# Kernel optimization log

Hardware: AMD Instinct MI355X
Metric: run time of the kernel (lower is better)

The kernel has to match this reference:

```python
import jax, jax.numpy as jnp
import numpy as np

H = W = 32
V = 1.5  # gaussian sigma used by the original _gussin(1.5)

def _gaussian_table():
    # gus[p, x, y] with p = i*32 + k, matching the original nested loops.
    r = np.arange(H, dtype=np.float64)
    d = (r[:, None, None, None] - r[None, None, :, None]) ** 2 \
        + (r[None, :, None, None] - r[None, None, None, :]) ** 2  # [i,k,x,y]
    g = np.exp(-d / (2.0 * V * V)) / (2.0 * np.pi * V * V)
    g = g.reshape(H * W, H, W)
    g = g / g.sum(axis=(1, 2), keepdims=True)  # per-position boundary normalization
    return jnp.asarray(g, dtype=jnp.float32)

_GUS = _gaussian_table()  # [1024, 32, 32]

def setup_inputs() -> dict:
    key = jax.random.key(0)
    ks = jax.random.split(key, 5)
    c, r = 1024, 16
    return {
        "x": jax.random.normal(ks[0], (1, c, H, W), jnp.float32),
        "se_w1": jax.random.normal(ks[1], (c // r, c), jnp.float32) * 0.03,
        "se_b1": jnp.zeros((c // r,), jnp.float32),
        "se_w2": jax.random.normal(ks[2], (c, c // r), jnp.float32) * 0.1,
        "se_b2": jnp.zeros((c,), jnp.float32),
        "conv_w": jax.random.normal(ks[3], (c, 2 * c), jnp.float32) * 0.02,
        "bn_gamma": jnp.ones((c,), jnp.float32),
        "bn_beta": jnp.zeros((c,), jnp.float32),
        "bn_mean": jnp.zeros((c,), jnp.float32),
        "bn_var": jnp.ones((c,), jnp.float32),
    }

def reference(x, se_w1, se_b1, se_w2, se_b2, conv_w, bn_gamma, bn_beta, bn_mean, bn_var):
    b, c, h, w = x.shape  # b == 1, h == w == 32 (hardcoded by the gaussian table)
    # ---- SE block ----
    y = x.mean(axis=(2, 3))                              # [b, c]
    y = jax.nn.relu(y @ se_w1.T + se_b1)                 # [b, c//r]
    y = jax.nn.sigmoid(y @ se_w2.T + se_b2)              # [b, c]
    x = x * y[:, :, None, None]
    # ---- gaussian spatial pooling (algebraic form of the O(H^2 W^2 C) expand) ----
    # x_spatial[c, p] = sum_{h,w} x[c,h,w] * gus[p,h,w]
    x_spatial = jnp.einsum('chw,phw->cp', x[0], _GUS).reshape(c, h, w)
    # ---- 3x3 local softmax attention on sigmoid features ----
    xr = jax.nn.sigmoid(x)                               # [1, c, h, w]
    xp = jnp.pad(xr, ((0, 0), (0, 0), (1, 1), (1, 1)))
    # torch F.unfold ordering: feature index = c_idx*9 + kh*3 + kw
    patches = jnp.stack([xp[:, :, i:i + h, j:j + w]
                         for i in range(3) for j in range(3)], axis=2)  # [1, c, 9, h, w]
    u = patches.reshape(c * 9, h * w).T                  # [hw, c*9]
    # faithful to the original reshape(hw, 3, 3, c) (reinterprets the c*9 layout)
    x3 = u.reshape(h * w, 3, 3, c)
    x1 = xr[0].transpose(1, 2, 0).reshape(h * w, 1, 1, c)
    logits = (x1 * x3).sum(-1).reshape(h * w, 9)         # [hw, 9]
    attn = jax.nn.softmax(logits, axis=1).reshape(h * w, 3, 3)
    x_range = jnp.einsum('pij,pijc->cp', attn, x3).reshape(c, h, w)
    # ---- fuse: 1x1 conv (no bias) + eval-mode BatchNorm + ReLU ----
    cat = jnp.concatenate([x_range, x_spatial], axis=0).reshape(b, 2 * c, h, w)
    out = jnp.einsum('oc,bchw->bohw', conv_w, cat)
    inv = jax.lax.rsqrt(bn_var + 1e-5)
    out = (out - bn_mean[None, :, None, None]) * (inv * bn_gamma)[None, :, None, None] \
          + bn_beta[None, :, None, None]
    return jax.nn.relu(out)
```

## Files before the change

kernel.cpp:

```cpp
#include <hip/hip_runtime.h>
#include <hip/hip_bf16.h>


typedef __attribute__((ext_vector_type(8))) short v8s;
typedef __attribute__((ext_vector_type(4))) float v4f;

__device__ __forceinline__ float sigmoidf_(float v) {
    return 1.f / (1.f + __expf(-v));
}
__device__ __forceinline__ unsigned short f2bf(float f) {
    unsigned u = __float_as_uint(f);
    u += 0x7fffu + ((u >> 16) & 1u);
    return (unsigned short)(u >> 16);
}
__device__ __forceinline__ float bf2f(unsigned short s) {
    return __uint_as_float(((unsigned)s) << 16);
}

__global__ __launch_bounds__(256) void k_A(const float* __restrict__ x,
                                           const float* __restrict__ W,
                                           const float* __restrict__ w1,
                                           const float* __restrict__ gamma,
                                           const float* __restrict__ beta,
                                           const float* __restrict__ mu,
                                           const float* __restrict__ var,
                                           unsigned short* __restrict__ Wb,
                                           unsigned short* __restrict__ U,
                                           float* __restrict__ zpart,
                                           float* __restrict__ bnsc,
                                           float* __restrict__ bnsh) {
    __shared__ unsigned short Gb[32 * 48];
    __shared__ unsigned short Xs[4][32 * 48];
    __shared__ unsigned short Ts[4][32 * 48];
    __shared__ float ms4[4];
    int tid = threadIdx.x, bx = blockIdx.x;
    int wv = tid >> 6, lane = tid & 63;
    {
        int row = tid >> 3, col0 = (tid & 7) << 2;
        float e[4], s = 0.f;
        #pragma unroll
        for (int j = 0; j < 4; ++j) {
            float d = (float)(row - (col0 + j));
            e[j] = __expf(-d * d / 4.5f);
            s += e[j];
        }
        s += __shfl_xor(s, 4, 8);
        s += __shfl_xor(s, 2, 8);
        s += __shfl_xor(s, 1, 8);
        float is = 1.f / s;
        uint2 pk;
        pk.x = (unsigned)f2bf(e[0] * is) | ((unsigned)f2bf(e[1] * is) << 16);
        pk.y = (unsigned)f2bf(e[2] * is) | ((unsigned)f2bf(e[3] * is) << 16);
        *(uint2*)&Gb[row * 48 + col0] = pk;
    }
    #pragma unroll
    for (int k = 0; k < 8; ++k) {
        int e = (k << 18) + (bx << 10) + (tid << 2);
        float4 v = *(const float4*)(W + e);
        uint2 pk;
        pk.x = (unsigned)f2bf(v.x) | ((unsigned)f2bf(v.y) << 16);
        pk.y = (unsigned)f2bf(v.z) | ((unsigned)f2bf(v.w) << 16);
        *(uint2*)(Wb + e) = pk;
    }
    int c = (bx << 2) + wv;
    if (lane == 0) {
        float iv = rsqrtf(var[c] + 1e-5f);
        float sc = iv * gamma[c];
        bnsc[c] = sc;
        bnsh[c] = beta[c] - mu[c] * sc;
    }
    const float* xp = x + (size_t)c * 1024;
    float4 vj[4];
    float s = 0.f;
    #pragma unroll
    for (int j = 0; j < 4; ++j) {
        vj[j] = *(const float4*)(xp + (j << 8) + (lane << 2));
        s += vj[j].x + vj[j].y + vj[j].z + vj[j].w;
    }
    #pragma unroll
    for (int o = 32; o; o >>= 1) s += __shfl_down(s, o);
    if (lane == 0) ms4[wv] = s * (1.f / 1024.f);
    #pragma unroll
    for (int j = 0; j < 4; ++j) {
        int h = (j << 3) + (lane >> 3);
        int w0 = (lane & 7) << 2;
        uint2 pk;
        pk.x = (unsigned)f2bf(vj[j].x) | ((unsigned)f2bf(vj[j].y) << 16);
        pk.y = (unsigned)f2bf(vj[j].z) | ((unsigned)f2bf(vj[j].w) << 16);
        *(uint2*)&Xs[wv][h * 48 + w0] = pk;
    }
    __syncthreads();
    int colf = lane & 15, quad = lane >> 4;
    v8s ga[2], xbv[2];
    #pragma unroll
    for (int mi = 0; mi < 2; ++mi)
        ga[mi] = *(const v8s*)&Gb[(mi * 16 + colf) * 48 + quad * 8];
    #pragma unroll
    for (int ni = 0; ni < 2; ++ni)
        xbv[ni] = *(const v8s*)&Xs[wv][(ni * 16 + colf) * 48 + quad * 8];
    v4f c1[2][2];
    #pragma unroll
    for (int mi = 0; mi < 2; ++mi)
        #pragma unroll
        for (int ni = 0; ni < 2; ++ni) {
            c1[mi][ni] = (v4f){0.f, 0.f, 0.f, 0.f};
            c1[mi][ni] = __builtin_amdgcn_mfma_f32_16x16x32_bf16(ga[mi], xbv[ni], c1[mi][ni], 0, 0, 0);
        }
    #pragma unroll
    for (int mi = 0; mi < 2; ++mi)
        #pragma unroll
        for (int ni = 0; ni < 2; ++ni)
            #pragma unroll
            for (int r = 0; r < 4; ++r)
                Ts[wv][(mi * 16 + quad * 4 + r) * 48 + ni * 16 + colf] = f2bf(c1[mi][ni][r]);
    __syncthreads();
    v8s tb[2];
    #pragma unroll
    for (int ni = 0; ni < 2; ++ni)
        tb[ni] = *(const v8s*)&Ts[wv][(ni * 16 + colf) * 48 + quad * 8];
    v4f c2[2][2];
    #pragma unroll
    for (int mi = 0; mi < 2; ++mi)
        #pragma unroll
        for (int ni = 0; ni < 2; ++ni) {
            c2[mi][ni] = (v4f){0.f, 0.f, 0.f, 0.f};
            c2[mi][ni] = __builtin_amdgcn_mfma_f32_16x16x32_bf16(ga[mi], tb[ni], c2[mi][ni], 0, 0, 0);
        }
    #pragma unroll
    for (int mi = 0; mi < 2; ++mi)
        #pragma unroll
        for (int ni = 0; ni < 2; ++ni)
            #pragma unroll
            for (int r = 0; r < 4; ++r)
                U[(size_t)c * 1024 + (mi * 16 + quad * 4 + r) * 32 + ni * 16 + colf] =
                    f2bf(c2[mi][ni][r]);
    if (wv == 0) {
        float4 wr = *(const float4*)(w1 + (size_t)lane * 1024 + (bx << 2));
        zpart[lane * 256 + bx] = wr.x * ms4[0] + wr.y * ms4[1]
                               + wr.z * ms4[2] + wr.w * ms4[3];
    }
}

__global__ __launch_bounds__(256) void k_prep(const float* __restrict__ x,
                                              const float* __restrict__ zpart,
                                              const float* __restrict__ b1,
                                              const float* __restrict__ w2,
                                              const float* __restrict__ b2,
                                              const unsigned short* __restrict__ U,
                                              unsigned short* __restrict__ xrb,
                                              unsigned short* __restrict__ Bt) {
    __shared__ float y1s[64];
    __shared__ float y2s[64];
    __shared__ float T[64][65];
    int tid = threadIdx.x;
    int p0 = blockIdx.x << 6, c0 = blockIdx.y << 6;
    {
        int j = tid >> 2, q = tid & 3;
        const float4* zp = (const float4*)(zpart + j * 256 + q * 64);
        float s = 0.f;
        #pragma unroll
        for (int i = 0; i < 16; ++i) {
            float4 v = zp[i];
            s += v.x + v.y + v.z + v.w;
        }
        s += __shfl_down(s, 2, 4);
        s += __shfl_down(s, 1, 4);
        if (q == 0) y1s[j] = fmaxf(s + b1[j], 0.f);
    }
    __syncthreads();
    {
        int ci = tid >> 2, sub = tid & 3;
        float s = 0.f;
        const float* w2r = w2 + (size_t)(c0 + ci) * 64 + sub * 16;
        #pragma unroll
        for (int i = 0; i < 4; ++i) {
            float4 wv4 = *(const float4*)(w2r + (i << 2));
            float4 yv4 = *(const float4*)&y1s[sub * 16 + (i << 2)];
            s += wv4.x * yv4.x + wv4.y * yv4.y + wv4.z * yv4.z + wv4.w * yv4.w;
        }
        s += __shfl_down(s, 2, 4);
        s += __shfl_down(s, 1, 4);
        if (sub == 0) y2s[ci] = sigmoidf_(s + b2[c0 + ci]);
    }
    __syncthreads();
    #pragma unroll
    for (int i = 0; i < 4; ++i) {
        int idx = tid + (i << 8);
        int row = idx >> 4;
        int col = (idx & 15) << 2;
        float sc = y2s[row];
        float4 v = *(const float4*)(x + (size_t)(c0 + row) * 1024 + p0 + col);
        T[col + 0][row] = sigmoidf_(v.x * sc);
        T[col + 1][row] = sigmoidf_(v.y * sc);
        T[col + 2][row] = sigmoidf_(v.z * sc);
        T[col + 3][row] = sigmoidf_(v.w * sc);
    }
    __syncthreads();
    #pragma unroll
    for (int i = 0; i < 4; ++i) {
        int idx = tid + (i << 8);
        int prow = idx >> 4;
        int cc = (idx & 15) << 2;
        uint2 pk;
        pk.x = (unsigned)f2bf(T[prow][cc + 0]) | ((unsigned)f2bf(T[prow][cc + 1]) << 16);
        pk.y = (unsigned)f2bf(T[prow][cc + 2]) | ((unsigned)f2bf(T[prow][cc + 3]) << 16);
        *(uint2*)(xrb + (size_t)(p0 + prow) * 1024 + c0 + cc) = pk;
    }
    __syncthreads();
    #pragma unroll
    for (int i = 0; i < 4; ++i) {
        int idx = tid + (i << 8);
        int row = idx >> 4;
        int col = (idx & 15) << 2;
        float sc = y2s[row];
        uint2 pk = *(const uint2*)(U + (size_t)(c0 + row) * 1024 + p0 + col);
        T[col + 0][row] = bf2f((unsigned short)(pk.x & 0xffffu)) * sc;
        T[col + 1][row] = bf2f((unsigned short)(pk.x >> 16)) * sc;
        T[col + 2][row] = bf2f((unsigned short)(pk.y & 0xffffu)) * sc;
        T[col + 3][row] = bf2f((unsigned short)(pk.y >> 16)) * sc;
    }
    __syncthreads();
    #pragma unroll
    for (int i = 0; i < 4; ++i) {
        int idx = tid + (i << 8);
        int prow = idx >> 4;
        int cc = (idx & 15) << 2;
        uint2 pk;
        pk.x = (unsigned)f2bf(T[prow][cc + 0]) | ((unsigned)f2bf(T[prow][cc + 1]) << 16);
        pk.y = (unsigned)f2bf(T[prow][cc + 2]) | ((unsigned)f2bf(T[prow][cc + 3]) << 16);
        *(uint2*)(Bt + (size_t)(p0 + prow) * 2048 + 1024 + c0 + cc) = pk;
    }
}

__global__ __launch_bounds__(256) void k_attn(const unsigned short* __restrict__ xrb,
                                              unsigned short* __restrict__ Bt) {
    __shared__ struct { unsigned short val[9216]; float part[9][4]; } sm;
    int tid = threadIdx.x;
    int p = blockIdx.x;
    int wv = tid >> 6, lane = tid & 63;
    int h = p >> 5, w = p & 31;
    float ctr[4];
    #pragma unroll
    for (int rem = 0; rem < 9; ++rem) {
        int dh = rem / 3 - 1, dw = rem % 3 - 1;
        bool ok = ((unsigned)(h + dh) < 32u) && ((unsigned)(w + dw) < 32u);
        uint2 v = make_uint2(0u, 0u);
        if (ok)
            v = *(const uint2*)(xrb + (size_t)((h + dh) * 32 + (w + dw)) * 1024 + 4 * tid);
        unsigned short e0 = (unsigned short)(v.x & 0xffffu);
        unsigned short e1 = (unsigned short)(v.x >> 16);
        unsigned short e2 = (unsigned short)(v.y & 0xffffu);
        unsigned short e3 = (unsigned short)(v.y >> 16);
        sm.val[(4 * tid + 0) * 9 + rem] = e0;
        sm.val[(4 * tid + 1) * 9 + rem] = e1;
        sm.val[(4 * tid + 2) * 9 + rem] = e2;
        sm.val[(4 * tid + 3) * 9 + rem] = e3;
        if (rem == 4) {
            ctr[0] = bf2f(e0); ctr[1] = bf2f(e1); ctr[2] = bf2f(e2); ctr[3] = bf2f(e3);
        }
    }
    __syncthreads();
    float vvq[9][4], lg[9];
    #pragma unroll
    for (int q = 0; q < 9; ++q) {
        uint2 pk = *(const uint2*)&sm.val[(q << 10) + 4 * tid];
        vvq[q][0] = bf2f((unsigned short)(pk.x & 0xffffu));
        vvq[q][1] = bf2f((unsigned short)(pk.x >> 16));
        vvq[q][2] = bf2f((unsigned short)(pk.y & 0xffffu));
        vvq[q][3] = bf2f((unsigned short)(pk.y >> 16));
        lg[q] = ctr[0] * vvq[q][0] + ctr[1] * vvq[q][1]
              + ctr[2] * vvq[q][2] + ctr[3] * vvq[q][3];
    }
    #pragma unroll
    for (int q = 0; q < 9; ++q) {
        float s = lg[q];
        #pragma unroll
        for (int o = 32; o; o >>= 1) s += __shfl_down(s, o);
        if (lane == 0) sm.part[q][wv] = s;
    }
    __syncthreads();
    float a9[9], mx = -3.4e38f;
    #pragma unroll
    for (int q = 0; q < 9; ++q) {
        a9[q] = sm.part[q][0] + sm.part[q][1] + sm.part[q][2] + sm.part[q][3];
        mx = fmaxf(mx, a9[q]);
    }
    float se = 0.f;
    #pragma unroll
    for (int q = 0; q < 9; ++q) { a9[q] = __expf(a9[q] - mx); se += a9[q]; }
    float inv = 1.f / se;
    float o4[4] = {0.f, 0.f, 0.f, 0.f};
    #pragma unroll
    for (int q = 0; q < 9; ++q) {
        float a = a9[q] * inv;
        #pragma unroll
        for (int j = 0; j < 4; ++j) o4[j] += a * vvq[q][j];
    }
    uint2 pk;
    pk.x = (unsigned)f2bf(o4[0]) | ((unsigned)f2bf(o4[1]) << 16);
    pk.y = (unsigned)f2bf(o4[2]) | ((unsigned)f2bf(o4[3]) << 16);
    *(uint2*)(Bt + (size_t)p * 2048 + 4 * tid) = pk;
}

__global__ __launch_bounds__(512) void k_main(
    const unsigned short* __restrict__ A, const unsigned short* __restrict__ B,
    float* __restrict__ outF,
    const float* __restrict__ bnsc, const float* __restrict__ bnsh) {
    __shared__ unsigned short As[2][64 * 136];
    __shared__ unsigned short Bs[2][64 * 136];
    const int K = 2048;
    int tid = threadIdx.x;
    int bid = blockIdx.x;
    int xcd = bid & 7, idx = bid >> 3;
    int by = ((xcd >> 1) << 2) + (idx >> 3);
    int bxn = ((xcd & 1) << 3) + (idx & 7);
    int m0 = by << 6, n0 = bxn << 6;
    int wv = tid >> 6, lane = tid & 63;
    int wm = wv & 3, wn = wv >> 2;
    int col = lane & 15, quad = lane >> 4;
    int srow = tid >> 3;
    int schunk = tid & 7;
    v4f acc[2];
    acc[0] = (v4f){0.f, 0.f, 0.f, 0.f};
    acc[1] = (v4f){0.f, 0.f, 0.f, 0.f};

    const float4* pa = (const float4*)(A + (size_t)(m0 + srow) * K + schunk * 8);
    const float4* pb = (const float4*)(B + (size_t)(n0 + srow) * K + schunk * 8);
    float4 ra0 = pa[0], ra1 = pa[8], rb0 = pb[0], rb1 = pb[8];
    *(float4*)&As[0][srow * 136 + schunk * 8] = ra0;
    *(float4*)&As[0][srow * 136 + schunk * 8 + 64] = ra1;
    *(float4*)&Bs[0][srow * 136 + schunk * 8] = rb0;
    *(float4*)&Bs[0][srow * 136 + schunk * 8 + 64] = rb1;
    for (int it = 0; it < 16; ++it) {
        __syncthreads();
        int cur = it & 1;
        if (it + 1 < 16) {
            int k0 = (it + 1) << 7;
            pa = (const float4*)(A + (size_t)(m0 + srow) * K + k0 + schunk * 8);
            pb = (const float4*)(B + (size_t)(n0 + srow) * K + k0 + schunk * 8);
            ra0 = pa[0]; ra1 = pa[8];
            rb0 = pb[0]; rb1 = pb[8];
        }
        #pragma unroll
        for (int ks = 0; ks < 4; ++ks) {
            int kg = ks * 4 + quad;
            int rA = wm * 16 + col;
            int rB = wn * 32 + col;
            v8s a  = *(const v8s*)&As[cur][rA * 136 + kg * 8];
            v8s b0 = *(const v8s*)&Bs[cur][rB * 136 + kg * 8];
            v8s b1 = *(const v8s*)&Bs[cur][(rB + 16) * 136 + kg * 8];
            acc[0] = __builtin_amdgcn_mfma_f32_16x16x32_bf16(a, b0, acc[0], 0, 0, 0);
            acc[1] = __builtin_amdgcn_mfma_f32_16x16x32_bf16(a, b1, acc[1], 0, 0, 0);
        }
        if (it + 1 < 16) {
            int nxt = cur ^ 1;
            *(float4*)&As[nxt][srow * 136 + schunk * 8] = ra0;
            *(float4*)&As[nxt][srow * 136 + schunk * 8 + 64] = ra1;
            *(float4*)&Bs[nxt][srow * 136 + schunk * 8] = rb0;
            *(float4*)&Bs[nxt][srow * 136 + schunk * 8 + 64] = rb1;
        }
    }
    #pragma unroll
    for (int ni = 0; ni < 2; ++ni) {
        int mb = m0 + wm * 16 + quad * 4;
        int nn = n0 + wn * 32 + ni * 16 + col;
        #pragma unroll
        for (int r = 0; r < 4; ++r) {
            int mm = mb + r;
            float sc = bnsc[mm];
            float sh = bnsh[mm];
            outF[((size_t)mm << 10) + nn] = fmaxf(fmaf(acc[ni][r], sc, sh), 0.f);
        }
    }
}

extern "C" void kernel_launch(void* const* d_in, const int* in_sizes, int n_in,
                              void* d_out, int out_size, void* d_ws, size_t ws_size,
                              hipStream_t stream) {
    const float* x     = (const float*)d_in[0];
    const float* w1    = (const float*)d_in[1];
    const float* b1    = (const float*)d_in[2];
    const float* w2    = (const float*)d_in[3];
    const float* b2    = (const float*)d_in[4];
    const float* cw    = (const float*)d_in[5];
    const float* gamma = (const float*)d_in[6];
    const float* beta  = (const float*)d_in[7];
    const float* mu    = (const float*)d_in[8];
    const float* var   = (const float*)d_in[9];
    float* wsf = (float*)d_ws;
    unsigned short* Wb  = (unsigned short*)wsf;
    unsigned short* Bt  = (unsigned short*)(wsf + (1 << 20));
    unsigned short* xrb = (unsigned short*)(wsf + (2 << 20));
    unsigned short* U   = (unsigned short*)(wsf + (2 << 20) + (1 << 19));
    float* zpart = wsf + (3 << 20);
    float* bnsc  = zpart + 16384;
    float* bnsh  = bnsc + 1024;
    float* out  = (float*)d_out;

    k_A    <<<256, 256, 0, stream>>>(x, cw, w1, gamma, beta, mu, var, Wb, U, zpart, bnsc, bnsh);
    k_prep <<<dim3(16, 16), 256, 0, stream>>>(x, zpart, b1, w2, b2, U, xrb, Bt);
    k_attn <<<1024, 256, 0, stream>>>(xrb, Bt);
    k_main <<<256, 512, 0, stream>>>(Wb, Bt, out, bnsc, bnsh);
}
```

Measured before the change: 112.6 us.

## Move weight bf16 conversion into attention kernel and split-K GEMM warps

The fp32-to-bf16 conversion of the conv weight moves out of k_A and into k_attn, where each of the 1024 blocks converts a 2048-element slice. This spreads the conversion over more blocks that are otherwise latency-bound. In k_main, each warp now computes a 32x32 output subtile over half of every K chunk (split-K across warp pairs) instead of 16x32 over the full chunk. This raises register-level reuse of A/B fragments per MFMA. The two K halves are summed through shared memory before the BN+ReLU epilogue, which adds an extra barrier and LDS traffic.

```diff
diff --git a/kernel.cpp b/kernel.cpp
--- a/kernel.cpp
+++ b/kernel.cpp
@@ -18,13 +18,11 @@
 }
 
 __global__ __launch_bounds__(256) void k_A(const float* __restrict__ x,
-                                           const float* __restrict__ W,
                                            const float* __restrict__ w1,
                                            const float* __restrict__ gamma,
                                            const float* __restrict__ beta,
                                            const float* __restrict__ mu,
                                            const float* __restrict__ var,
-                                           unsigned short* __restrict__ Wb,
                                            unsigned short* __restrict__ U,
                                            float* __restrict__ zpart,
                                            float* __restrict__ bnsc,
@@ -52,15 +50,6 @@
         pk.x = (unsigned)f2bf(e[0] * is) | ((unsigned)f2bf(e[1] * is) << 16);
         pk.y = (unsigned)f2bf(e[2] * is) | ((unsigned)f2bf(e[3] * is) << 16);
         *(uint2*)&Gb[row * 48 + col0] = pk;
-    }
-    #pragma unroll
-    for (int k = 0; k < 8; ++k) {
-        int e = (k << 18) + (bx << 10) + (tid << 2);
-        float4 v = *(const float4*)(W + e);
-        uint2 pk;
-        pk.x = (unsigned)f2bf(v.x) | ((unsigned)f2bf(v.y) << 16);
-        pk.y = (unsigned)f2bf(v.z) | ((unsigned)f2bf(v.w) << 16);
-        *(uint2*)(Wb + e) = pk;
     }
     int c = (bx << 2) + wv;
     if (lane == 0) {
@@ -233,12 +222,26 @@
 }
 
 __global__ __launch_bounds__(256) void k_attn(const unsigned short* __restrict__ xrb,
+                                              const float* __restrict__ W,
+                                              unsigned short* __restrict__ Wb,
                                               unsigned short* __restrict__ Bt) {
     __shared__ struct { unsigned short val[9216]; float part[9][4]; } sm;
     int tid = threadIdx.x;
     int p = blockIdx.x;
     int wv = tid >> 6, lane = tid & 63;
     int h = p >> 5, w = p & 31;
+    {
+        int e0 = (p << 11) + (tid << 2);
+        float4 v0 = *(const float4*)(W + e0);
+        float4 v1 = *(const float4*)(W + e0 + 1024);
+        uint2 pk0, pk1;
+        pk0.x = (unsigned)f2bf(v0.x) | ((unsigned)f2bf(v0.y) << 16);
+        pk0.y = (unsigned)f2bf(v0.z) | ((unsigned)f2bf(v0.w) << 16);
+        pk1.x = (unsigned)f2bf(v1.x) | ((unsigned)f2bf(v1.y) << 16);
+        pk1.y = (unsigned)f2bf(v1.z) | ((unsigned)f2bf(v1.w) << 16);
+        *(uint2*)(Wb + e0) = pk0;
+        *(uint2*)(Wb + e0 + 1024) = pk1;
+    }
     float ctr[4];
     #pragma unroll
     for (int rem = 0; rem < 9; ++rem) {
@@ -316,13 +319,15 @@
     int bxn = ((xcd & 1) << 3) + (idx & 7);
     int m0 = by << 6, n0 = bxn << 6;
     int wv = tid >> 6, lane = tid & 63;
-    int wm = wv & 3, wn = wv >> 2;
+    int wk = wv & 1, wm = (wv >> 1) & 1, wn = wv >> 2;
     int col = lane & 15, quad = lane >> 4;
     int srow = tid >> 3;
     int schunk = tid & 7;
-    v4f acc[2];
-    acc[0] = (v4f){0.f, 0.f, 0.f, 0.f};
-    acc[1] = (v4f){0.f, 0.f, 0.f, 0.f};
+    v4f acc[2][2];
+    #pragma unroll
+    for (int i = 0; i < 2; ++i)
+        #pragma unroll
+        for (int j = 0; j < 2; ++j) acc[i][j] = (v4f){0.f, 0.f, 0.f, 0.f};
 
     const float4* pa = (const float4*)(A + (size_t)(m0 + srow) * K + schunk * 8);
     const float4* pb = (const float4*)(B + (size_t)(n0 + srow) * K + schunk * 8);
@@ -342,15 +347,18 @@
             rb0 = pb[0]; rb1 = pb[8];
         }
         #pragma unroll
-        for (int ks = 0; ks < 4; ++ks) {
-            int kg = ks * 4 + quad;
-            int rA = wm * 16 + col;
+        for (int ks = 0; ks < 2; ++ks) {
+            int kg = wk * 8 + ks * 4 + quad;
+            int rA = wm * 32 + col;
             int rB = wn * 32 + col;
-            v8s a  = *(const v8s*)&As[cur][rA * 136 + kg * 8];
+            v8s a0 = *(const v8s*)&As[cur][rA * 136 + kg * 8];
+            v8s a1 = *(const v8s*)&As[cur][(rA + 16) * 136 + kg * 8];
             v8s b0 = *(const v8s*)&Bs[cur][rB * 136 + kg * 8];
             v8s b1 = *(const v8s*)&Bs[cur][(rB + 16) * 136 + kg * 8];
-            acc[0] = __builtin_amdgcn_mfma_f32_16x16x32_bf16(a, b0, acc[0], 0, 0, 0);
-            acc[1] = __builtin_amdgcn_mfma_f32_16x16x32_bf16(a, b1, acc[1], 0, 0, 0);
+            acc[0][0] = __builtin_amdgcn_mfma_f32_16x16x32_bf16(a0, b0, acc[0][0], 0, 0, 0);
+            acc[0][1] = __builtin_amdgcn_mfma_f32_16x16x32_bf16(a0, b1, acc[0][1], 0, 0, 0);
+            acc[1][0] = __builtin_amdgcn_mfma_f32_16x16x32_bf16(a1, b0, acc[1][0], 0, 0, 0);
+            acc[1][1] = __builtin_amdgcn_mfma_f32_16x16x32_bf16(a1, b1, acc[1][1], 0, 0, 0);
         }
         if (it + 1 < 16) {
             int nxt = cur ^ 1;
@@ -360,17 +368,34 @@
             *(float4*)&Bs[nxt][srow * 136 + schunk * 8 + 64] = rb1;
         }
     }
-    #pragma unroll
-    for (int ni = 0; ni < 2; ++ni) {
-        int mb = m0 + wm * 16 + quad * 4;
-        int nn = n0 + wn * 32 + ni * 16 + col;
-        #pragma unroll
-        for (int r = 0; r < 4; ++r) {
-            int mm = mb + r;
-            float sc = bnsc[mm];
-            float sh = bnsh[mm];
-            outF[((size_t)mm << 10) + nn] = fmaxf(fmaf(acc[ni][r], sc, sh), 0.f);
-        }
+    float* scr = (float*)&As[0][0];
+    int pair = wm * 2 + wn;
+    if (wk == 1) {
+        #pragma unroll
+        for (int mi = 0; mi < 2; ++mi)
+            #pragma unroll
+            for (int ni = 0; ni < 2; ++ni)
+                #pragma unroll
+                for (int r = 0; r < 4; ++r)
+                    scr[pair * 1056 + (mi * 16 + quad * 4 + r) * 33 + ni * 16 + col] =
+                        acc[mi][ni][r];
+    }
+    __syncthreads();
+    if (wk == 0) {
+        #pragma unroll
+        for (int mi = 0; mi < 2; ++mi)
+            #pragma unroll
+            for (int ni = 0; ni < 2; ++ni) {
+                int mb = m0 + wm * 32 + mi * 16 + quad * 4;
+                int nn = n0 + wn * 32 + ni * 16 + col;
+                #pragma unroll
+                for (int r = 0; r < 4; ++r) {
+                    int mm = mb + r;
+                    float v = acc[mi][ni][r]
+                            + scr[pair * 1056 + (mi * 16 + quad * 4 + r) * 33 + ni * 16 + col];
+                    outF[((size_t)mm << 10) + nn] = fmaxf(fmaf(v, bnsc[mm], bnsh[mm]), 0.f);
+                }
+            }
     }
 }
 
@@ -397,8 +422,8 @@
     float* bnsh  = bnsc + 1024;
     float* out  = (float*)d_out;
 
-    k_A    <<<256, 256, 0, stream>>>(x, cw, w1, gamma, beta, mu, var, Wb, U, zpart, bnsc, bnsh);
+    k_A    <<<256, 256, 0, stream>>>(x, w1, gamma, beta, mu, var, U, zpart, bnsc, bnsh);
     k_prep <<<dim3(16, 16), 256, 0, stream>>>(x, zpart, b1, w2, b2, U, xrb, Bt);
-    k_attn <<<1024, 256, 0, stream>>>(xrb, Bt);
+    k_attn <<<1024, 256, 0, stream>>>(xrb, cw, Wb, Bt);
     k_main <<<256, 512, 0, stream>>>(Wb, Bt, out, bnsc, bnsh);
 }
```

Result: no change. 114.1 us (+1.3%).
